# Optimization experiments

Hardware: AMD Instinct MI355X
Metric: run time of the kernel (lower is better)

The kernel has to match this reference:

```python
import jax, jax.numpy as jnp
import numpy as np

INPUT_DIM = 1024
OUTPUT_DIM = 1000
DEPTH = 10
LAMBDA_REG = 1e-3
N_INTERNAL = 2 ** DEPTH - 1
N_LEAF = 2 ** DEPTH
BATCH = 16384


def setup_inputs() -> dict:
    key = jax.random.key(0)
    k1, k2, k3 = jax.random.split(key, 3)
    X = jax.random.normal(k1, (BATCH, INPUT_DIM), dtype=jnp.float32)
    # torch nn.Linear weight layout: [out_features, in_features]; scaled to keep
    # sigmoid routing probs away from 0/1 saturation (log-reg term).
    W_internal = jax.random.normal(k2, (N_INTERNAL, INPUT_DIM + 1), dtype=jnp.float32) * 0.02
    W_leaf = jax.random.normal(k3, (OUTPUT_DIM, N_LEAF), dtype=jnp.float32) * 0.02
    return {"X": X, "W_internal": W_internal, "W_leaf": W_leaf}


def _tree_paths(X, W_internal):
    B = X.shape[0]
    Xb = jnp.concatenate([jnp.ones((B, 1), X.dtype), X], axis=1)  # [B, D+1]
    logits = jax.nn.sigmoid(Xb @ W_internal.T)                    # [B, N_int]
    routing = jnp.stack([logits, 1.0 - logits], axis=2)           # [B, N_int, 2]
    path = jnp.ones((B, 1), X.dtype)
    reg = jnp.float32(0.0)
    start = 0
    for layer in range(DEPTH):
        n = 2 ** layer
        lp = routing[:, start:start + n, :].reshape(B, 2 * n)     # next_paths [B, 2n]
        path = jnp.repeat(path, 2, axis=1) * lp                   # new path probs [B, 2n]
        # Faithful to source: parent_idx = node_idx // 2 indexes the UPDATED path probs.
        parent = jnp.repeat(path[:, :n], 2, axis=1)               # [B, 2n]
        num = jnp.sum(lp * parent, axis=0)                        # [2n]
        den = jnp.sum(parent, axis=0) + 1e-8                      # [2n]
        alpha = num / den
        factor = LAMBDA_REG * 2.0 ** (-layer)
        reg = reg + factor * jnp.sum(-0.5 * (jnp.log(alpha) + jnp.log(1.0 - alpha)))
        start += n
    return path, reg  # path: [B, 2^DEPTH]


def reference(X, W_internal, W_leaf):
    path_probs, reg = _tree_paths(X, W_internal)
    predictions = path_probs @ W_leaf.T   # [B, output_dim]
    return predictions, reg
```

## Files before the change

### kernel.cpp

```cpp
#include <hip/hip_runtime.h>
#include <hip/hip_bf16.h>

#define B_ROWS 16384
#define K_DIM  1024
#define N_INT  1023
#define N_OUT  1000

using s8vec = __attribute__((ext_vector_type(8))) short;
using f32x4 = __attribute__((ext_vector_type(4))) float;

static const size_t OFF_XB   = 0;
static const size_t OFF_W1   = OFF_XB   + 33554432;
static const size_t OFF_BIAS = OFF_W1   + 2097152;
static const size_t OFF_PROB = OFF_BIAS + 4096;
static const size_t OFF_PATH = OFF_PROB + 33554432;
static const size_t OFF_W2   = OFF_PATH + 33554432;
static const size_t OFF_S1   = OFF_W2   + 2097152;
static const size_t OFF_S2   = OFF_S1   + 4096;

__device__ __forceinline__ float b2f(ushort u) {
  return __uint_as_float(((unsigned)u) << 16);
}
__device__ __forceinline__ ushort f2b(float f) {
  unsigned u = __float_as_uint(f);
  u = u + 0x7FFFu + ((u >> 16) & 1u);
  return (ushort)(u >> 16);
}

__global__ __launch_bounds__(256) void cvt_x(const float4* __restrict__ X,
                                             ushort4* __restrict__ O) {
  const int i = blockIdx.x * 256 + threadIdx.x;
  const float4 v = X[i];
  ushort4 o;
  o.x = f2b(v.x); o.y = f2b(v.y); o.z = f2b(v.z); o.w = f2b(v.w);
  O[i] = o;
}

__global__ __launch_bounds__(256) void cvt_w1(const float* __restrict__ W,
                                              ushort* __restrict__ W1,
                                              float* __restrict__ bias) {
  const int idx = blockIdx.x * 256 + threadIdx.x;
  const int n = idx >> 10, k = idx & 1023;
  const float v = (n < N_INT) ? W[n * 1025 + 1 + k] : 0.f;
  W1[idx] = f2b(v);
  if (k == 0) bias[n] = (n < N_INT) ? W[n * 1025] : 0.f;
}

__global__ __launch_bounds__(256) void cvt_w2(const float* __restrict__ W,
                                              ushort* __restrict__ W2) {
  const int idx = blockIdx.x * 256 + threadIdx.x;
  const int n = idx >> 10, k = idx & 1023;
  const float v = (n < N_OUT) ? W[n * 1024 + k] : 0.f;
  W2[idx] = f2b(v);
}

template <int MODE>
__global__ __launch_bounds__(256) void gemm_bt(const ushort* __restrict__ A,
                                               const ushort* __restrict__ Bm,
                                               const float* __restrict__ bias,
                                               void* __restrict__ outp) {
  __shared__ ushort As[4096];
  __shared__ ushort Bs[4096];
  const int tid = threadIdx.x;
  const int bn = blockIdx.x, bm = blockIdx.y;
  const int lane = tid & 63, wv = tid >> 6;
  const int wm = wv >> 1, wn = wv & 1;
  const int m16 = lane & 15, q = lane >> 4;

  const ushort* a0p = A  + (size_t)(bm * 128 + (tid >> 2)) * 1024 + (tid & 3) * 8;
  const ushort* b0p = Bm + (size_t)(bn * 128 + (tid >> 2)) * 1024 + (tid & 3) * 8;

  f32x4 acc[4][4] = {};

  for (int k0 = 0; k0 < 1024; k0 += 32) {
    *(uint4*)(As + tid * 8)        = *(const uint4*)(a0p + k0);
    *(uint4*)(As + 2048 + tid * 8) = *(const uint4*)(a0p + 65536 + k0);
    *(uint4*)(Bs + tid * 8)        = *(const uint4*)(b0p + k0);
    *(uint4*)(Bs + 2048 + tid * 8) = *(const uint4*)(b0p + 65536 + k0);
    __syncthreads();
    s8vec af[4], bfv[4];
#pragma unroll
    for (int i = 0; i < 4; ++i)
      af[i] = *(const s8vec*)(As + (wm * 64 + i * 16 + m16) * 32 + q * 8);
#pragma unroll
    for (int j = 0; j < 4; ++j)
      bfv[j] = *(const s8vec*)(Bs + (wn * 64 + j * 16 + m16) * 32 + q * 8);
#pragma unroll
    for (int i = 0; i < 4; ++i)
#pragma unroll
      for (int j = 0; j < 4; ++j)
        acc[i][j] = __builtin_amdgcn_mfma_f32_16x16x32_bf16(af[i], bfv[j], acc[i][j], 0, 0, 0);
    __syncthreads();
  }

  if (MODE == 0) {
    ushort* P = (ushort*)outp;
#pragma unroll
    for (int i = 0; i < 4; ++i)
#pragma unroll
      for (int r = 0; r < 4; ++r) {
        const int gr = bm * 128 + wm * 64 + i * 16 + q * 4 + r;
#pragma unroll
        for (int j = 0; j < 4; ++j) {
          const int gc = bn * 128 + wn * 64 + j * 16 + m16;
          const float z = acc[i][j][r] + bias[gc];
          const float p = 1.f / (1.f + expf(-z));
          P[(size_t)gr * 1024 + gc] = f2b(p);
        }
      }
  } else {
    float* O = (float*)outp;
#pragma unroll
    for (int i = 0; i < 4; ++i)
#pragma unroll
      for (int r = 0; r < 4; ++r) {
        const int gr = bm * 128 + wm * 64 + i * 16 + q * 4 + r;
#pragma unroll
        for (int j = 0; j < 4; ++j) {
          const int gc = bn * 128 + wn * 64 + j * 16 + m16;
          if (gc < N_OUT) O[(size_t)gr * 1000 + gc] = acc[i][j][r];
        }
      }
  }
}

__global__ __launch_bounds__(256) void tree_kernel(const ushort* __restrict__ probs,
                                                   ushort* __restrict__ path,
                                                   float* __restrict__ S1g,
                                                   float* __restrict__ S2g) {
  __shared__ float S1s[1023];
  __shared__ float S2s[1023];
  for (int i = threadIdx.x; i < 1023; i += 256) { S1s[i] = 0.f; S2s[i] = 0.f; }
  __syncthreads();
  const int lane = threadIdx.x & 63;
  const int gw = blockIdx.x * 4 + (threadIdx.x >> 6);

  float at1[6] = {}, at2[6] = {};
  float ae1[30] = {}, ae2[30] = {};

  for (int r = gw; r < B_ROWS; r += 1024) {
    const ushort* prow = probs + (size_t)r * 1024;
    float v = 1.f;
#pragma unroll
    for (int t = 1; t <= 6; ++t) {
      const int ell = t - 1;
      const int e = lane >> (6 - t);
      const float p = b2f(prow[(1 << ell) - 1 + (e >> 1)]);
      v *= (e & 1) ? (1.f - p) : p;
      if (((lane & ((1 << (6 - t)) - 1)) == 0) && (e < (1 << ell))) {
        const float pj = b2f(prow[(1 << ell) - 1 + e]);
        at1[ell] += v;
        at2[ell] += pj * v;
      }
    }
    float w[16];
    w[0] = v;
#pragma unroll
    for (int ell = 6; ell <= 9; ++ell) {
      const int s = 1 << (ell - 6);
      const int pb = (1 << ell) - 1;
#pragma unroll
      for (int i = s - 1; i >= 0; --i) {
        const float p = b2f(prow[pb + s * lane + i]);
        w[2 * i + 1] = w[i] * (1.f - p);
        w[2 * i]     = w[i] * p;
      }
      if (lane < 32) {
        const int base = 2 * s - 2;
#pragma unroll
        for (int i = 0; i < 2 * s; ++i) {
          const int j = 2 * s * lane + i;
          const float pj = b2f(prow[pb + j]);
          ae1[base + i] += w[i];
          ae2[base + i] += pj * w[i];
        }
      }
    }
    union { ushort u[16]; uint4 q4[2]; } pk;
#pragma unroll
    for (int i = 0; i < 16; ++i) pk.u[i] = f2b(w[i]);
    uint4* dst = (uint4*)(path + (size_t)r * 1024 + lane * 16);
    dst[0] = pk.q4[0];
    dst[1] = pk.q4[1];
  }

#pragma unroll
  for (int t = 1; t <= 6; ++t) {
    const int ell = t - 1;
    const int e = lane >> (6 - t);
    if (((lane & ((1 << (6 - t)) - 1)) == 0) && (e < (1 << ell))) {
      atomicAdd(&S1s[(1 << ell) - 1 + e], at1[ell]);
      atomicAdd(&S2s[(1 << ell) - 1 + e], at2[ell]);
    }
  }
  if (lane < 32) {
#pragma unroll
    for (int ell = 6; ell <= 9; ++ell) {
      const int s = 1 << (ell - 6);
      const int pb = (1 << ell) - 1;
      const int base = 2 * s - 2;
#pragma unroll
      for (int i = 0; i < 2 * s; ++i) {
        atomicAdd(&S1s[pb + 2 * s * lane + i], ae1[base + i]);
        atomicAdd(&S2s[pb + 2 * s * lane + i], ae2[base + i]);
      }
    }
  }
  __syncthreads();
  for (int i = threadIdx.x; i < 1023; i += 256) {
    atomicAdd(&S1g[i], S1s[i]);
    atomicAdd(&S2g[i], S2s[i]);
  }
}

__global__ __launch_bounds__(1024) void finalize_kernel(const float* __restrict__ S1g,
                                                        const float* __restrict__ S2g,
                                                        float* __restrict__ outreg) {
  const int tid = threadIdx.x;
  double val = 0.0;
  if (tid < 1023) {
    const int ell = 31 - __clz(tid + 1);
    const double s1 = (double)S1g[tid];
    const double s2 = (double)S2g[tid];
    const double den = s1 + 1e-8;
    const double a0 = s2 / den;
    const double a1 = (s1 - s2) / den;
    const double f = 1e-3 * (1.0 / (double)(1 << ell));
    val = -0.5 * f * (log(a0) + log(1.0 - a0) + log(a1) + log(1.0 - a1));
  }
#pragma unroll
  for (int o = 32; o > 0; o >>= 1) val += __shfl_down(val, o, 64);
  __shared__ double part[16];
  if ((tid & 63) == 0) part[tid >> 6] = val;
  __syncthreads();
  if (tid == 0) {
    double t = 0.0;
    for (int i = 0; i < 16; ++i) t += part[i];
    outreg[0] = (float)t;
  }
}

extern "C" void kernel_launch(void* const* d_in, const int* in_sizes, int n_in,
                              void* d_out, int out_size, void* d_ws, size_t ws_size,
                              hipStream_t stream) {
  const float* X     = (const float*)d_in[0];
  const float* Wint  = (const float*)d_in[1];
  const float* Wleaf = (const float*)d_in[2];
  float* out = (float*)d_out;
  char* ws = (char*)d_ws;

  ushort* Xb   = (ushort*)(ws + OFF_XB);
  ushort* W1   = (ushort*)(ws + OFF_W1);
  float*  bias = (float*)(ws + OFF_BIAS);
  ushort* prob = (ushort*)(ws + OFF_PROB);
  ushort* path = (ushort*)(ws + OFF_PATH);
  ushort* W2   = (ushort*)(ws + OFF_W2);
  float*  S1g  = (float*)(ws + OFF_S1);
  float*  S2g  = (float*)(ws + OFF_S2);

  (void)hipMemsetAsync(ws + OFF_S1, 0, 8192, stream);
  cvt_x<<<16384, 256, 0, stream>>>((const float4*)X, (ushort4*)Xb);
  cvt_w1<<<4096, 256, 0, stream>>>(Wint, W1, bias);
  cvt_w2<<<4096, 256, 0, stream>>>(Wleaf, W2);
  gemm_bt<0><<<dim3(8, 128), 256, 0, stream>>>(Xb, W1, bias, (void*)prob);
  tree_kernel<<<256, 256, 0, stream>>>(prob, path, S1g, S2g);
  gemm_bt<1><<<dim3(8, 128), 256, 0, stream>>>(path, W2, nullptr, (void*)out);
  finalize_kernel<<<1, 1024, 0, stream>>>(S1g, S2g, out + (size_t)B_ROWS * N_OUT);
}
```

Measured before the change: 334.2 us.

## Use direct global-to-LDS loads in GEMM and vectorize tree kernel row loads

The GEMM main loop now uses global_load_lds to copy tiles straight into shared memory instead of staging them through registers. The probability matrix is stored shifted by one column so that each tree level starts at a power-of-two offset. This lets the tree kernel read each level with one wide vector load per lane and redistribute values with shuffles instead of many scalar loads. The tree kernel also gets more blocks, and global atomics are replaced with per-block partial sums written to workspace and reduced by a new kernel, which removes the memset. It costs an extra launch and about 16 MB of partial-sum traffic, and it reuses the Xb workspace region, which is safe only because Xb is dead by then.

```diff
diff --git a/kernel.cpp b/kernel.cpp
--- a/kernel.cpp
+++ b/kernel.cpp
@@ -10,21 +10,30 @@
 using f32x4 = __attribute__((ext_vector_type(4))) float;
 
 static const size_t OFF_XB   = 0;
+static const size_t OFF_PART = 0;
+static const size_t OFF_SG   = 16777216;
 static const size_t OFF_W1   = OFF_XB   + 33554432;
 static const size_t OFF_BIAS = OFF_W1   + 2097152;
 static const size_t OFF_PROB = OFF_BIAS + 4096;
 static const size_t OFF_PATH = OFF_PROB + 33554432;
 static const size_t OFF_W2   = OFF_PATH + 33554432;
-static const size_t OFF_S1   = OFF_W2   + 2097152;
-static const size_t OFF_S2   = OFF_S1   + 4096;
 
 __device__ __forceinline__ float b2f(ushort u) {
   return __uint_as_float(((unsigned)u) << 16);
 }
+__device__ __forceinline__ float blo(unsigned u) { return __uint_as_float(u << 16); }
+__device__ __forceinline__ float bhi(unsigned u) { return __uint_as_float(u & 0xffff0000u); }
 __device__ __forceinline__ ushort f2b(float f) {
   unsigned u = __float_as_uint(f);
   u = u + 0x7FFFu + ((u >> 16) & 1u);
   return (ushort)(u >> 16);
+}
+
+__device__ __forceinline__ void gload16(const void* g, void* l) {
+  __builtin_amdgcn_global_load_lds(
+      (const __attribute__((address_space(1))) void*)g,
+      (__attribute__((address_space(3))) void*)l,
+      16, 0, 0);
 }
 
 __global__ __launch_bounds__(256) void cvt_x(const float4* __restrict__ X,
@@ -69,14 +78,16 @@
 
   const ushort* a0p = A  + (size_t)(bm * 128 + (tid >> 2)) * 1024 + (tid & 3) * 8;
   const ushort* b0p = Bm + (size_t)(bn * 128 + (tid >> 2)) * 1024 + (tid & 3) * 8;
+  ushort* As_w = As + wv * 512;
+  ushort* Bs_w = Bs + wv * 512;
 
   f32x4 acc[4][4] = {};
 
   for (int k0 = 0; k0 < 1024; k0 += 32) {
-    *(uint4*)(As + tid * 8)        = *(const uint4*)(a0p + k0);
-    *(uint4*)(As + 2048 + tid * 8) = *(const uint4*)(a0p + 65536 + k0);
-    *(uint4*)(Bs + tid * 8)        = *(const uint4*)(b0p + k0);
-    *(uint4*)(Bs + 2048 + tid * 8) = *(const uint4*)(b0p + 65536 + k0);
+    gload16(a0p + k0,         As_w);
+    gload16(a0p + 65536 + k0, As_w + 2048);
+    gload16(b0p + k0,         Bs_w);
+    gload16(b0p + 65536 + k0, Bs_w + 2048);
     __syncthreads();
     s8vec af[4], bfv[4];
 #pragma unroll
@@ -105,7 +116,7 @@
           const int gc = bn * 128 + wn * 64 + j * 16 + m16;
           const float z = acc[i][j][r] + bias[gc];
           const float p = 1.f / (1.f + expf(-z));
-          P[(size_t)gr * 1024 + gc] = f2b(p);
+          if (gc < N_INT) P[(size_t)gr * 1024 + gc + 1] = f2b(p);
         }
       }
   } else {
@@ -126,11 +137,9 @@
 
 __global__ __launch_bounds__(256) void tree_kernel(const ushort* __restrict__ probs,
                                                    ushort* __restrict__ path,
-                                                   float* __restrict__ S1g,
-                                                   float* __restrict__ S2g) {
-  __shared__ float S1s[1023];
-  __shared__ float S2s[1023];
-  for (int i = threadIdx.x; i < 1023; i += 256) { S1s[i] = 0.f; S2s[i] = 0.f; }
+                                                   float* __restrict__ part) {
+  __shared__ float Ss[4096];
+  for (int i = threadIdx.x; i < 4096; i += 256) Ss[i] = 0.f;
   __syncthreads();
   const int lane = threadIdx.x & 63;
   const int gw = blockIdx.x * 4 + (threadIdx.x >> 6);
@@ -138,41 +147,106 @@
   float at1[6] = {}, at2[6] = {};
   float ae1[30] = {}, ae2[30] = {};
 
-  for (int r = gw; r < B_ROWS; r += 1024) {
+#pragma unroll 1
+  for (int rr = 0; rr < 4; ++rr) {
+    const int r = gw * 4 + rr;
     const ushort* prow = probs + (size_t)r * 1024;
+    const ushort p6 = prow[64 + lane];
+    const uint   p7 = *(const uint*)(prow + 128 + 2 * lane);
+    const uint2  p8 = *(const uint2*)(prow + 256 + 4 * lane);
+    const uint4  p9 = *(const uint4*)(prow + 512 + 8 * lane);
+
     float v = 1.f;
 #pragma unroll
     for (int t = 1; t <= 6; ++t) {
       const int ell = t - 1;
       const int e = lane >> (6 - t);
-      const float p = b2f(prow[(1 << ell) - 1 + (e >> 1)]);
+      const float p = b2f(prow[(1 << ell) + (e >> 1)]);
       v *= (e & 1) ? (1.f - p) : p;
       if (((lane & ((1 << (6 - t)) - 1)) == 0) && (e < (1 << ell))) {
-        const float pj = b2f(prow[(1 << ell) - 1 + e]);
+        const float pj = b2f(prow[(1 << ell) + e]);
         at1[ell] += v;
         at2[ell] += pj * v;
       }
     }
+
     float w[16];
-    w[0] = v;
-#pragma unroll
-    for (int ell = 6; ell <= 9; ++ell) {
-      const int s = 1 << (ell - 6);
-      const int pb = (1 << ell) - 1;
-#pragma unroll
-      for (int i = s - 1; i >= 0; --i) {
-        const float p = b2f(prow[pb + s * lane + i]);
+    {
+      const float p = b2f(p6);
+      w[1] = v * (1.f - p); w[0] = v * p;
+    }
+    {
+      const int j0 = __shfl((int)p6, 2 * lane);
+      const int j1 = __shfl((int)p6, 2 * lane + 1);
+      if (lane < 32) {
+        ae1[0] += w[0]; ae2[0] += b2f((ushort)j0) * w[0];
+        ae1[1] += w[1]; ae2[1] += b2f((ushort)j1) * w[1];
+      }
+    }
+    {
+      const float pA = blo(p7), pB = bhi(p7);
+      w[3] = w[1] * (1.f - pB); w[2] = w[1] * pB;
+      w[1] = w[0] * (1.f - pA); w[0] = w[0] * pA;
+    }
+    {
+      const uint ua = (uint)__shfl((int)p7, 2 * lane);
+      const uint ub = (uint)__shfl((int)p7, 2 * lane + 1);
+      if (lane < 32) {
+        ae1[2] += w[0]; ae2[2] += blo(ua) * w[0];
+        ae1[3] += w[1]; ae2[3] += bhi(ua) * w[1];
+        ae1[4] += w[2]; ae2[4] += blo(ub) * w[2];
+        ae1[5] += w[3]; ae2[5] += bhi(ub) * w[3];
+      }
+    }
+    {
+      const float pv[4] = { blo(p8.x), bhi(p8.x), blo(p8.y), bhi(p8.y) };
+#pragma unroll
+      for (int i = 3; i >= 0; --i) {
+        w[2 * i + 1] = w[i] * (1.f - pv[i]);
+        w[2 * i]     = w[i] * pv[i];
+      }
+    }
+    {
+      const uint u0 = (uint)__shfl((int)p8.x, 2 * lane);
+      const uint u1 = (uint)__shfl((int)p8.y, 2 * lane);
+      const uint u2 = (uint)__shfl((int)p8.x, 2 * lane + 1);
+      const uint u3 = (uint)__shfl((int)p8.y, 2 * lane + 1);
+      if (lane < 32) {
+        ae1[6]  += w[0]; ae2[6]  += blo(u0) * w[0];
+        ae1[7]  += w[1]; ae2[7]  += bhi(u0) * w[1];
+        ae1[8]  += w[2]; ae2[8]  += blo(u1) * w[2];
+        ae1[9]  += w[3]; ae2[9]  += bhi(u1) * w[3];
+        ae1[10] += w[4]; ae2[10] += blo(u2) * w[4];
+        ae1[11] += w[5]; ae2[11] += bhi(u2) * w[5];
+        ae1[12] += w[6]; ae2[12] += blo(u3) * w[6];
+        ae1[13] += w[7]; ae2[13] += bhi(u3) * w[7];
+      }
+    }
+    {
+      const uint pv[4] = { p9.x, p9.y, p9.z, p9.w };
+#pragma unroll
+      for (int i = 7; i >= 0; --i) {
+        const float p = (i & 1) ? bhi(pv[i >> 1]) : blo(pv[i >> 1]);
         w[2 * i + 1] = w[i] * (1.f - p);
         w[2 * i]     = w[i] * p;
       }
+    }
+    {
+      uint s_[8];
+      s_[0] = (uint)__shfl((int)p9.x, 2 * lane);
+      s_[1] = (uint)__shfl((int)p9.y, 2 * lane);
+      s_[2] = (uint)__shfl((int)p9.z, 2 * lane);
+      s_[3] = (uint)__shfl((int)p9.w, 2 * lane);
+      s_[4] = (uint)__shfl((int)p9.x, 2 * lane + 1);
+      s_[5] = (uint)__shfl((int)p9.y, 2 * lane + 1);
+      s_[6] = (uint)__shfl((int)p9.z, 2 * lane + 1);
+      s_[7] = (uint)__shfl((int)p9.w, 2 * lane + 1);
       if (lane < 32) {
-        const int base = 2 * s - 2;
-#pragma unroll
-        for (int i = 0; i < 2 * s; ++i) {
-          const int j = 2 * s * lane + i;
-          const float pj = b2f(prow[pb + j]);
-          ae1[base + i] += w[i];
-          ae2[base + i] += pj * w[i];
+#pragma unroll
+        for (int i = 0; i < 16; ++i) {
+          const uint u = s_[i >> 1];
+          const float pj = (i & 1) ? bhi(u) : blo(u);
+          ae1[14 + i] += w[i]; ae2[14 + i] += pj * w[i];
         }
       }
     }
@@ -189,8 +263,9 @@
     const int ell = t - 1;
     const int e = lane >> (6 - t);
     if (((lane & ((1 << (6 - t)) - 1)) == 0) && (e < (1 << ell))) {
-      atomicAdd(&S1s[(1 << ell) - 1 + e], at1[ell]);
-      atomicAdd(&S2s[(1 << ell) - 1 + e], at2[ell]);
+      const int node = (1 << ell) - 1 + e;
+      atomicAdd(&Ss[node], at1[ell]);
+      atomicAdd(&Ss[2048 + node], at2[ell]);
     }
   }
   if (lane < 32) {
@@ -201,27 +276,38 @@
       const int base = 2 * s - 2;
 #pragma unroll
       for (int i = 0; i < 2 * s; ++i) {
-        atomicAdd(&S1s[pb + 2 * s * lane + i], ae1[base + i]);
-        atomicAdd(&S2s[pb + 2 * s * lane + i], ae2[base + i]);
+        const int node = pb + 2 * s * lane + i;
+        atomicAdd(&Ss[node], ae1[base + i]);
+        atomicAdd(&Ss[2048 + node], ae2[base + i]);
       }
     }
   }
   __syncthreads();
-  for (int i = threadIdx.x; i < 1023; i += 256) {
-    atomicAdd(&S1g[i], S1s[i]);
-    atomicAdd(&S2g[i], S2s[i]);
-  }
-}
-
-__global__ __launch_bounds__(1024) void finalize_kernel(const float* __restrict__ S1g,
-                                                        const float* __restrict__ S2g,
+  float* prow_out = part + (size_t)blockIdx.x * 4096;
+  for (int i = threadIdx.x; i < 4096; i += 256) prow_out[i] = Ss[i];
+}
+
+__global__ __launch_bounds__(256) void reduce_kernel(const float* __restrict__ part,
+                                                     float* __restrict__ Sg) {
+  const int t = blockIdx.x * 256 + threadIdx.x;
+  float s0 = 0.f, s1 = 0.f, s2 = 0.f, s3 = 0.f;
+  for (int b = 0; b < 1024; b += 4) {
+    s0 += part[(size_t)(b + 0) * 4096 + t];
+    s1 += part[(size_t)(b + 1) * 4096 + t];
+    s2 += part[(size_t)(b + 2) * 4096 + t];
+    s3 += part[(size_t)(b + 3) * 4096 + t];
+  }
+  Sg[t] = (s0 + s1) + (s2 + s3);
+}
+
+__global__ __launch_bounds__(1024) void finalize_kernel(const float* __restrict__ Sg,
                                                         float* __restrict__ outreg) {
   const int tid = threadIdx.x;
   double val = 0.0;
   if (tid < 1023) {
     const int ell = 31 - __clz(tid + 1);
-    const double s1 = (double)S1g[tid];
-    const double s2 = (double)S2g[tid];
+    const double s1 = (double)Sg[tid];
+    const double s2 = (double)Sg[2048 + tid];
     const double den = s1 + 1e-8;
     const double a0 = s2 / den;
     const double a1 = (s1 - s2) / den;
@@ -230,12 +316,12 @@
   }
 #pragma unroll
   for (int o = 32; o > 0; o >>= 1) val += __shfl_down(val, o, 64);
-  __shared__ double part[16];
-  if ((tid & 63) == 0) part[tid >> 6] = val;
+  __shared__ double partd[16];
+  if ((tid & 63) == 0) partd[tid >> 6] = val;
   __syncthreads();
   if (tid == 0) {
     double t = 0.0;
-    for (int i = 0; i < 16; ++i) t += part[i];
+    for (int i = 0; i < 16; ++i) t += partd[i];
     outreg[0] = (float)t;
   }
 }
@@ -255,15 +341,15 @@
   ushort* prob = (ushort*)(ws + OFF_PROB);
   ushort* path = (ushort*)(ws + OFF_PATH);
   ushort* W2   = (ushort*)(ws + OFF_W2);
-  float*  S1g  = (float*)(ws + OFF_S1);
-  float*  S2g  = (float*)(ws + OFF_S2);
-
-  (void)hipMemsetAsync(ws + OFF_S1, 0, 8192, stream);
+  float*  part = (float*)(ws + OFF_PART);
+  float*  Sg   = (float*)(ws + OFF_SG);
+
   cvt_x<<<16384, 256, 0, stream>>>((const float4*)X, (ushort4*)Xb);
   cvt_w1<<<4096, 256, 0, stream>>>(Wint, W1, bias);
   cvt_w2<<<4096, 256, 0, stream>>>(Wleaf, W2);
   gemm_bt<0><<<dim3(8, 128), 256, 0, stream>>>(Xb, W1, bias, (void*)prob);
-  tree_kernel<<<256, 256, 0, stream>>>(prob, path, S1g, S2g);
+  tree_kernel<<<1024, 256, 0, stream>>>(prob, path, part);
   gemm_bt<1><<<dim3(8, 128), 256, 0, stream>>>(path, W2, nullptr, (void*)out);
-  finalize_kernel<<<1, 1024, 0, stream>>>(S1g, S2g, out + (size_t)B_ROWS * N_OUT);
-}
+  reduce_kernel<<<16, 256, 0, stream>>>(part, Sg);
+  finalize_kernel<<<1, 1024, 0, stream>>>(Sg, out + (size_t)B_ROWS * N_OUT);
+}
```

Result: slower. 402.4 us (+20.4%).
